# Performance work log

Measured on AMD Instinct MI355X. Metric: run time of the kernel, lower is better.

## Reference

```python
import jax, jax.numpy as jnp
import numpy as np

B, E, L = 262144, 16, 224  # pixels, endmembers, spectral bands


def setup_inputs() -> dict:
    key = jax.random.key(0)
    kx, ke, kb = jax.random.split(key, 3)
    x = jax.random.uniform(kx, (B, E), dtype=jnp.float32)          # abundances
    endmembers = jax.random.uniform(ke, (E, L), dtype=jnp.float32)  # spectral signatures
    b_s = jax.random.normal(kb, (B,), dtype=jnp.float32) * 0.1      # per-pixel PPNM coeff
    return {"x": x, "endmembers": endmembers, "b_s": b_s}


def reference(x, endmembers, b_s):
    # mat = x @ W : [B, L]
    mat = jnp.matmul(x, endmembers)
    # Original: mat + transpose(matmul(transpose(mat*mat), diag(b_s)))
    # which is exactly a row-wise scale of mat^2 by b_s.
    return mat + b_s[:, None] * (mat * mat)
```

## Files before the change

### kernel.cpp

```cpp
#include <hip/hip_runtime.h>


#define LBANDS 224
#define EMEMB  16
#define GROUPS 56
#define PPHASE 8
#define NTHREADS (GROUPS * PPHASE)
#define PPB    32
#define XCHUNKS (PPB * 4)

__global__ __launch_bounds__(NTHREADS, 4) void ppnm_kernel(
    const float* __restrict__ x,
    const float* __restrict__ w,
    const float* __restrict__ bs,
    float* __restrict__ out,
    int B)
{
    const int t  = threadIdx.x;
    const int g  = t % GROUPS;
    const int pw = t / GROUPS;

    float4 Wf[EMEMB];
    #pragma unroll
    for (int k = 0; k < EMEMB; ++k) {
        Wf[k] = *reinterpret_cast<const float4*>(w + k * LBANDS + 4 * g);
    }

    __shared__ float4 xsh[2][XCHUNKS];
    __shared__ float  bsh[2][PPB];

    const int bodies  = B / PPB;
    const int bstride = gridDim.x;

    int body = blockIdx.x;
    if (body >= bodies) return;

    const float4* xv = reinterpret_cast<const float4*>(x);

    if (t < XCHUNKS) {
        xsh[0][t] = xv[body * XCHUNKS + t];
    } else if (t < XCHUNKS + PPB) {
        bsh[0][t - XCHUNKS] = bs[body * PPB + (t - XCHUNKS)];
    }
    __syncthreads();

#define PPNM_FMA4(SCAL, K)                                                    \
        acc.x = fmaf((SCAL), Wf[K].x, acc.x);                                 \
        acc.y = fmaf((SCAL), Wf[K].y, acc.y);                                 \
        acc.z = fmaf((SCAL), Wf[K].z, acc.z);                                 \
        acc.w = fmaf((SCAL), Wf[K].w, acc.w);

    int cur = 0;
    for (;;) {
        const int nbody     = body + bstride;
        const bool have_next = (nbody < bodies);

        float4 xstage = make_float4(0.f, 0.f, 0.f, 0.f);
        float  bstage = 0.f;
        if (have_next) {
            if (t < XCHUNKS) {
                xstage = xv[nbody * XCHUNKS + t];
            } else if (t < XCHUNKS + PPB) {
                bstage = bs[nbody * PPB + (t - XCHUNKS)];
            }
        }

        #pragma unroll
        for (int j = 0; j < PPB / PPHASE; ++j) {
            const int px = pw + PPHASE * j;
            const float4 xa = xsh[cur][px * 4 + 0];
            const float4 xb = xsh[cur][px * 4 + 1];
            const float4 xc = xsh[cur][px * 4 + 2];
            const float4 xd = xsh[cur][px * 4 + 3];
            const float  sb = bsh[cur][px];

            float4 acc = make_float4(0.f, 0.f, 0.f, 0.f);
            PPNM_FMA4(xa.x,  0) PPNM_FMA4(xa.y,  1)
            PPNM_FMA4(xa.z,  2) PPNM_FMA4(xa.w,  3)
            PPNM_FMA4(xb.x,  4) PPNM_FMA4(xb.y,  5)
            PPNM_FMA4(xb.z,  6) PPNM_FMA4(xb.w,  7)
            PPNM_FMA4(xc.x,  8) PPNM_FMA4(xc.y,  9)
            PPNM_FMA4(xc.z, 10) PPNM_FMA4(xc.w, 11)
            PPNM_FMA4(xd.x, 12) PPNM_FMA4(xd.y, 13)
            PPNM_FMA4(xd.z, 14) PPNM_FMA4(xd.w, 15)

            float4 r;
            r.x = fmaf(sb * acc.x, acc.x, acc.x);
            r.y = fmaf(sb * acc.y, acc.y, acc.y);
            r.z = fmaf(sb * acc.z, acc.z, acc.z);
            r.w = fmaf(sb * acc.w, acc.w, acc.w);

            *reinterpret_cast<float4*>(out + (body * PPB + px) * LBANDS + 4 * g) = r;
        }

        if (!have_next) break;

        if (t < XCHUNKS) {
            xsh[cur ^ 1][t] = xstage;
        } else if (t < XCHUNKS + PPB) {
            bsh[cur ^ 1][t - XCHUNKS] = bstage;
        }
        __syncthreads();

        body = nbody;
        cur ^= 1;
    }

#undef PPNM_FMA4
}

extern "C" void kernel_launch(void* const* d_in, const int* in_sizes, int n_in,
                              void* d_out, int out_size, void* d_ws, size_t ws_size,
                              hipStream_t stream) {
    const float* x  = (const float*)d_in[0];
    const float* w  = (const float*)d_in[1];
    const float* bs = (const float*)d_in[2];
    float* out = (float*)d_out;

    const int B = in_sizes[2];

    const int grid = 2048;
    ppnm_kernel<<<grid, NTHREADS, 0, stream>>>(x, w, bs, out, B);
}
```

Before: 257.2 us.

## Replace persistent double-buffered loop with one large tile per block

Removes the grid-stride persistent loop and its double-buffered shared-memory prefetch. Each block now processes a single 128-pixel tile, and the grid is sized to cover all pixels. Global loads of x and b_s are issued before the W register loads to overlap their latency. This drops per-iteration barriers and loop overhead, but relies on inter-block concurrency rather than in-block prefetching to hide memory latency.

```diff
diff --git a/kernel.cpp b/kernel.cpp
--- a/kernel.cpp
+++ b/kernel.cpp
@@ -6,7 +6,7 @@
 #define GROUPS 56
 #define PPHASE 8
 #define NTHREADS (GROUPS * PPHASE)
-#define PPB    32
+#define PPB    128
 #define XCHUNKS (PPB * 4)
 
 __global__ __launch_bounds__(NTHREADS, 4) void ppnm_kernel(
@@ -20,28 +20,30 @@
     const int g  = t % GROUPS;
     const int pw = t / GROUPS;
 
+    const int body = blockIdx.x;
+    if (body * PPB >= B) return;
+
+    __shared__ float4 xsh[XCHUNKS];
+    __shared__ float  bsh[PPB];
+
+    const float4* xv = reinterpret_cast<const float4*>(x);
+    const float4  v0 = xv[body * XCHUNKS + t];
+    float4 v1 = make_float4(0.f, 0.f, 0.f, 0.f);
+    if (t < XCHUNKS - NTHREADS)
+        v1 = xv[body * XCHUNKS + NTHREADS + t];
+    float bv = 0.f;
+    if (t < PPB)
+        bv = bs[body * PPB + t];
+
     float4 Wf[EMEMB];
     #pragma unroll
     for (int k = 0; k < EMEMB; ++k) {
         Wf[k] = *reinterpret_cast<const float4*>(w + k * LBANDS + 4 * g);
     }
 
-    __shared__ float4 xsh[2][XCHUNKS];
-    __shared__ float  bsh[2][PPB];
-
-    const int bodies  = B / PPB;
-    const int bstride = gridDim.x;
-
-    int body = blockIdx.x;
-    if (body >= bodies) return;
-
-    const float4* xv = reinterpret_cast<const float4*>(x);
-
-    if (t < XCHUNKS) {
-        xsh[0][t] = xv[body * XCHUNKS + t];
-    } else if (t < XCHUNKS + PPB) {
-        bsh[0][t - XCHUNKS] = bs[body * PPB + (t - XCHUNKS)];
-    }
+    xsh[t] = v0;
+    if (t < XCHUNKS - NTHREADS) xsh[NTHREADS + t] = v1;
+    if (t < PPB)                bsh[t] = bv;
     __syncthreads();
 
 #define PPNM_FMA4(SCAL, K)                                                    \
@@ -50,60 +52,32 @@
         acc.z = fmaf((SCAL), Wf[K].z, acc.z);                                 \
         acc.w = fmaf((SCAL), Wf[K].w, acc.w);
 
-    int cur = 0;
-    for (;;) {
-        const int nbody     = body + bstride;
-        const bool have_next = (nbody < bodies);
+    #pragma unroll
+    for (int j = 0; j < PPB / PPHASE; ++j) {
+        const int px = pw + PPHASE * j;
+        const float4 xa = xsh[px * 4 + 0];
+        const float4 xb = xsh[px * 4 + 1];
+        const float4 xc = xsh[px * 4 + 2];
+        const float4 xd = xsh[px * 4 + 3];
+        const float  sb = bsh[px];
 
-        float4 xstage = make_float4(0.f, 0.f, 0.f, 0.f);
-        float  bstage = 0.f;
-        if (have_next) {
-            if (t < XCHUNKS) {
-                xstage = xv[nbody * XCHUNKS + t];
-            } else if (t < XCHUNKS + PPB) {
-                bstage = bs[nbody * PPB + (t - XCHUNKS)];
-            }
-        }
+        float4 acc = make_float4(0.f, 0.f, 0.f, 0.f);
+        PPNM_FMA4(xa.x,  0) PPNM_FMA4(xa.y,  1)
+        PPNM_FMA4(xa.z,  2) PPNM_FMA4(xa.w,  3)
+        PPNM_FMA4(xb.x,  4) PPNM_FMA4(xb.y,  5)
+        PPNM_FMA4(xb.z,  6) PPNM_FMA4(xb.w,  7)
+        PPNM_FMA4(xc.x,  8) PPNM_FMA4(xc.y,  9)
+        PPNM_FMA4(xc.z, 10) PPNM_FMA4(xc.w, 11)
+        PPNM_FMA4(xd.x, 12) PPNM_FMA4(xd.y, 13)
+        PPNM_FMA4(xd.z, 14) PPNM_FMA4(xd.w, 15)
 
-        #pragma unroll
-        for (int j = 0; j < PPB / PPHASE; ++j) {
-            const int px = pw + PPHASE * j;
-            const float4 xa = xsh[cur][px * 4 + 0];
-            const float4 xb = xsh[cur][px * 4 + 1];
-            const float4 xc = xsh[cur][px * 4 + 2];
-            const float4 xd = xsh[cur][px * 4 + 3];
-            const float  sb = bsh[cur][px];
+        float4 r;
+        r.x = fmaf(sb * acc.x, acc.x, acc.x);
+        r.y = fmaf(sb * acc.y, acc.y, acc.y);
+        r.z = fmaf(sb * acc.z, acc.z, acc.z);
+        r.w = fmaf(sb * acc.w, acc.w, acc.w);
 
-            float4 acc = make_float4(0.f, 0.f, 0.f, 0.f);
-            PPNM_FMA4(xa.x,  0) PPNM_FMA4(xa.y,  1)
-            PPNM_FMA4(xa.z,  2) PPNM_FMA4(xa.w,  3)
-            PPNM_FMA4(xb.x,  4) PPNM_FMA4(xb.y,  5)
-            PPNM_FMA4(xb.z,  6) PPNM_FMA4(xb.w,  7)
-            PPNM_FMA4(xc.x,  8) PPNM_FMA4(xc.y,  9)
-            PPNM_FMA4(xc.z, 10) PPNM_FMA4(xc.w, 11)
-            PPNM_FMA4(xd.x, 12) PPNM_FMA4(xd.y, 13)
-            PPNM_FMA4(xd.z, 14) PPNM_FMA4(xd.w, 15)
-
-            float4 r;
-            r.x = fmaf(sb * acc.x, acc.x, acc.x);
-            r.y = fmaf(sb * acc.y, acc.y, acc.y);
-            r.z = fmaf(sb * acc.z, acc.z, acc.z);
-            r.w = fmaf(sb * acc.w, acc.w, acc.w);
-
-            *reinterpret_cast<float4*>(out + (body * PPB + px) * LBANDS + 4 * g) = r;
-        }
-
-        if (!have_next) break;
-
-        if (t < XCHUNKS) {
-            xsh[cur ^ 1][t] = xstage;
-        } else if (t < XCHUNKS + PPB) {
-            bsh[cur ^ 1][t - XCHUNKS] = bstage;
-        }
-        __syncthreads();
-
-        body = nbody;
-        cur ^= 1;
+        *reinterpret_cast<float4*>(out + (body * PPB + px) * LBANDS + 4 * g) = r;
     }
 
 #undef PPNM_FMA4
@@ -119,6 +93,6 @@
 
     const int B = in_sizes[2];
 
-    const int grid = 2048;
+    const int grid = (B + PPB - 1) / PPB;
     ppnm_kernel<<<grid, NTHREADS, 0, stream>>>(x, w, bs, out, B);
 }
```

After: 245.2 us (median of 2 runs). 1.05x faster.
